# Performance work log

Measured on AMD Instinct MI355X. Metric: run time of the kernel, lower is better.

## Reference

```python
import jax, jax.numpy as jnp
import numpy as np

EPSILON = 0.1
ALPHA = 0.5
N_ITER = 10
B, N, D, N_USERS = 4096, 4096, 16, 100000


def setup_inputs() -> dict:
    key = jax.random.key(0)
    k1, k2, k3, k4, k5, k6 = jax.random.split(key, 6)
    users_tensor = jax.random.randint(k1, (B,), 0, N_USERS)
    pois_tensor = jax.random.randint(k2, (B, N), 0, N)
    D_tensor = jax.random.uniform(k3, (B, N), dtype=jnp.float32)
    # ScaledEmbedding: normal init scaled by 1/embedding_dim
    poi_emb = jax.random.normal(k4, (N, D), dtype=jnp.float32) / D
    user_emb = jax.random.normal(k5, (N_USERS, D), dtype=jnp.float32) / D
    capacities = jax.random.uniform(k6, (N,), dtype=jnp.float32) + 0.5
    return {"users_tensor": users_tensor, "pois_tensor": pois_tensor,
            "D_tensor": D_tensor, "poi_emb": poi_emb,
            "user_emb": user_emb, "capacities": capacities}


def reference(users_tensor, pois_tensor, D_tensor, poi_emb, user_emb, capacities):
    pe = poi_emb[pois_tensor]            # [B, N, D]
    ue = user_emb[users_tensor]          # [B, D]
    dot = jnp.einsum('bnd,bd->bn', pe, ue)   # [B, N]
    affinity = (1.0 - ALPHA) * dot - ALPHA * (D_tensor / jnp.mean(D_tensor))
    K = jnp.exp(affinity / EPSILON)      # [B, N]
    a = jnp.ones((B,), dtype=K.dtype)
    b = capacities

    def body(i, uv):
        u, v = uv
        u = a / (K @ v)        # [B]
        v = b / (K.T @ u)      # [N]
        return (u, v)

    u0 = jnp.ones((B,), dtype=K.dtype)
    v0 = jnp.ones((N,), dtype=K.dtype)
    u, v = jax.lax.fori_loop(0, N_ITER, body, (u0, v0))
    P = K * (u[:, None] * v[None, :])    # [B, N]
    return P
```

## Files before the change

kernel.cpp:

```cpp
#include <hip/hip_runtime.h>
#include <hip/hip_fp16.h>

#define BB 4096
#define NN 4096
#define RPB 4
#define RPI 8
#define NBLK (BB / RPI)
#define NTSLOT 60

__device__ __forceinline__ int swzK(int bid) { return (bid & 7) * 128 + (bid >> 3); }

typedef float vf4 __attribute__((ext_vector_type(4)));
typedef int   vi4 __attribute__((ext_vector_type(4)));
__device__ __forceinline__ float4 ntl4(const float4* p) {
    vf4 r = __builtin_nontemporal_load((const vf4*)p);
    return *(float4*)&r;
}
__device__ __forceinline__ int4 ntl4i(const int4* p) {
    vi4 r = __builtin_nontemporal_load((const vi4*)p);
    return *(int4*)&r;
}
__device__ __forceinline__ void nts4(float4* p, float4 v) {
    __builtin_nontemporal_store(*(vf4*)&v, (vf4*)p);
}

__global__ __launch_bounds__(256) void k_mean(
        const float* __restrict__ Dt, float* __restrict__ dsum,
        float* __restrict__ v) {
    const int tid = blockIdx.x * blockDim.x + threadIdx.x;
    const int gs = gridDim.x * blockDim.x;
    if (tid < NN) v[tid] = 1.0f;
    const float4* D4 = (const float4*)Dt;
    const int total4 = (BB * NN) / 4;
    float s = 0.f;
    for (int i = tid; i < total4; i += gs) {
        float4 d = ntl4(&D4[i]);
        s += (d.x + d.y) + (d.z + d.w);
    }
    #pragma unroll
    for (int off = 32; off > 0; off >>= 1) s += __shfl_down(s, off, 64);
    __shared__ float ls[4];
    if ((threadIdx.x & 63) == 0) ls[threadIdx.x >> 6] = s;
    __syncthreads();
    if (threadIdx.x == 0) atomicAdd(dsum, (ls[0] + ls[1]) + (ls[2] + ls[3]));
}

__global__ __launch_bounds__(256) void k_K(
        const int* __restrict__ users, const int* __restrict__ pois,
        const float* __restrict__ Dt, const float* __restrict__ poi_emb,
        const float* __restrict__ user_emb, const float* __restrict__ dsum,
        __half* __restrict__ K) {
    __shared__ __half slut[RPB][NN];
    __shared__ float ues[RPB * 16];
    const int t = threadIdx.x;
    const int b0 = swzK(blockIdx.x) * RPB;
    if (t < RPB * 16) {
        int r = t >> 4, d = t & 15;
        ues[t] = user_emb[(size_t)users[b0 + r] * 16 + d];
    }
    __syncthreads();
    float ue[RPB][16];
    #pragma unroll
    for (int r = 0; r < RPB; r++)
        #pragma unroll
        for (int d = 0; d < 16; d++) ue[r][d] = ues[r * 16 + d];

    const float4* pe4 = (const float4*)poi_emb;
    for (int j = t; j < NN; j += 256) {
        float4 p0 = pe4[j * 4 + 0];
        float4 p1 = pe4[j * 4 + 1];
        float4 p2 = pe4[j * 4 + 2];
        float4 p3 = pe4[j * 4 + 3];
        #pragma unroll
        for (int r = 0; r < RPB; r++) {
            float acc = p0.x*ue[r][0]  + p0.y*ue[r][1]  + p0.z*ue[r][2]  + p0.w*ue[r][3]
                      + p1.x*ue[r][4]  + p1.y*ue[r][5]  + p1.z*ue[r][6]  + p1.w*ue[r][7]
                      + p2.x*ue[r][8]  + p2.y*ue[r][9]  + p2.z*ue[r][10] + p2.w*ue[r][11]
                      + p3.x*ue[r][12] + p3.y*ue[r][13] + p3.z*ue[r][14] + p3.w*ue[r][15];
            slut[r][j] = __float2half(acc);
        }
    }
    __syncthreads();
    const float cc = 5.0f * 16777216.0f / dsum[0];
    #pragma unroll
    for (int r = 0; r < RPB; r++) {
        const size_t base = (size_t)(b0 + r) * NN;
        const int4*   p4 = (const int4*)(pois + base);
        const float4* d4 = (const float4*)(Dt + base);
        #pragma unroll
        for (int i = 0; i < NN / 4 / 256; i++) {
            const int q = t + i * 256;
            int4   ci = ntl4i(&p4[q]);
            float4 cd = ntl4(&d4[q]);
            float k0 = __expf(5.0f * __half2float(slut[r][ci.x]) - cc * cd.x);
            float k1 = __expf(5.0f * __half2float(slut[r][ci.y]) - cc * cd.y);
            float k2 = __expf(5.0f * __half2float(slut[r][ci.z]) - cc * cd.z);
            float k3 = __expf(5.0f * __half2float(slut[r][ci.w]) - cc * cd.w);
            __half2* kw = (__half2*)&K[base + 4 * (size_t)q];
            kw[0] = __floats2half2_rn(k0, k1);
            kw[1] = __floats2half2_rn(k2, k3);
        }
    }
}

__global__ __launch_bounds__(512) void k_it(
        const __half* __restrict__ K, const float* __restrict__ v,
        float* __restrict__ part, float* __restrict__ u) {
    const int t = threadIdx.x;
    const int slot = blockIdx.x >> 3;
    const int sb = (blockIdx.x & 7) * 64 + slot;
    const int r0 = sb * RPI;
    const bool nt = (slot >= NTSLOT);

    const float4* w4 = (const float4*)v;
    float4 w0 = w4[2 * t], w1 = w4[2 * t + 1];

    float4 h[RPI];
    #pragma unroll
    for (int r = 0; r < RPI; r++) {
        const float4* p = (const float4*)(K + (size_t)(r0 + r) * NN) + t;
        h[r] = nt ? ntl4(p) : *p;
    }

    float acc[RPI];
    #pragma unroll
    for (int r = 0; r < RPI; r++) {
        const __half2* a = (const __half2*)&h[r];
        float2 f; float s = 0.f;
        f = __half22float2(a[0]); s += f.x * w0.x + f.y * w0.y;
        f = __half22float2(a[1]); s += f.x * w0.z + f.y * w0.w;
        f = __half22float2(a[2]); s += f.x * w1.x + f.y * w1.y;
        f = __half22float2(a[3]); s += f.x * w1.z + f.y * w1.w;
        acc[r] = s;
    }
    #pragma unroll
    for (int off = 32; off > 0; off >>= 1)
        #pragma unroll
        for (int r = 0; r < RPI; r++) acc[r] += __shfl_down(acc[r], off, 64);
    __shared__ float ls[8][RPI];
    __shared__ float us[RPI];
    if ((t & 63) == 0)
        #pragma unroll
        for (int r = 0; r < RPI; r++) ls[t >> 6][r] = acc[r];
    __syncthreads();
    if (t < RPI) {
        float s = 0.f;
        #pragma unroll
        for (int wv = 0; wv < 8; wv++) s += ls[wv][t];
        float uu = 1.0f / s;
        us[t] = uu;
        u[r0 + t] = uu;
    }
    __syncthreads();

    float4 A0 = make_float4(0, 0, 0, 0), A1 = A0;
    #pragma unroll
    for (int r = 0; r < RPI; r++) {
        const float ur = us[r];
        const __half2* a = (const __half2*)&h[r];
        float2 f;
        f = __half22float2(a[0]); A0.x += ur * f.x; A0.y += ur * f.y;
        f = __half22float2(a[1]); A0.z += ur * f.x; A0.w += ur * f.y;
        f = __half22float2(a[2]); A1.x += ur * f.x; A1.y += ur * f.y;
        f = __half22float2(a[3]); A1.z += ur * f.x; A1.w += ur * f.y;
    }
    float4* p4 = (float4*)(part + (size_t)sb * NN);
    nts4(&p4[2 * t],     A0);
    nts4(&p4[2 * t + 1], A1);
}

__global__ __launch_bounds__(256) void k_red(
        const float* __restrict__ part, const float* __restrict__ cap,
        float* __restrict__ v) {
    const int t = threadIdx.x;
    const int g = blockIdx.x;
    const int j = t & 7;
    const int s = t >> 3;
    const float4* p4 = (const float4*)part;
    float4 a = make_float4(0, 0, 0, 0);
    #pragma unroll
    for (int i = 0; i < NBLK / 32; i++) {
        float4 x = ntl4(&p4[(size_t)(s + 32 * i) * (NN / 4) + g * 8 + j]);
        a.x += x.x; a.y += x.y; a.z += x.z; a.w += x.w;
    }
    __shared__ float4 red[32][8];
    red[s][j] = a;
    __syncthreads();
    if (t < 8) {
        float4 b = red[0][t];
        #pragma unroll
        for (int s2 = 1; s2 < 32; s2++) {
            float4 x = red[s2][t];
            b.x += x.x; b.y += x.y; b.z += x.z; b.w += x.w;
        }
        float4 cc = ((const float4*)cap)[g * 8 + t];
        ((float4*)v)[g * 8 + t] =
            make_float4(cc.x / b.x, cc.y / b.y, cc.z / b.z, cc.w / b.w);
    }
}

__global__ __launch_bounds__(256) void k_P(
        const __half* __restrict__ K, const float* __restrict__ u,
        const float* __restrict__ v, float* __restrict__ P) {
    const int t = threadIdx.x;
    const int slot = blockIdx.x >> 3;
    const int sb = (blockIdx.x & 7) * 64 + slot;
    const int r0 = sb * RPI;
    const bool nt = (slot >= NTSLOT);
    const float4* v4 = (const float4*)v;
    float4 va0 = v4[2 * t],       va1 = v4[2 * t + 1];
    float4 vb0 = v4[512 + 2 * t], vb1 = v4[512 + 2 * t + 1];
    #pragma unroll 2
    for (int r = 0; r < RPI; r++) {
        const int b = r0 + r;
        const float ub = u[b];
        const size_t base = (size_t)b * NN;
        const float4* k4 = (const float4*)(K + base);
        float4 raw0 = nt ? ntl4(&k4[t])       : k4[t];
        float4 raw1 = nt ? ntl4(&k4[256 + t]) : k4[256 + t];
        const __half2* ha = (const __half2*)&raw0;
        const __half2* hb = (const __half2*)&raw1;
        float2 f0 = __half22float2(ha[0]);
        float2 f1 = __half22float2(ha[1]);
        float2 f2 = __half22float2(ha[2]);
        float2 f3 = __half22float2(ha[3]);
        float2 g0 = __half22float2(hb[0]);
        float2 g1 = __half22float2(hb[1]);
        float2 g2 = __half22float2(hb[2]);
        float2 g3 = __half22float2(hb[3]);
        float4* P4 = (float4*)(P + base);
        nts4(&P4[2*t],       make_float4(f0.x*ub*va0.x, f0.y*ub*va0.y, f1.x*ub*va0.z, f1.y*ub*va0.w));
        nts4(&P4[2*t+1],     make_float4(f2.x*ub*va1.x, f2.y*ub*va1.y, f3.x*ub*va1.z, f3.y*ub*va1.w));
        nts4(&P4[512+2*t],   make_float4(g0.x*ub*vb0.x, g0.y*ub*vb0.y, g1.x*ub*vb0.z, g1.y*ub*vb0.w));
        nts4(&P4[512+2*t+1], make_float4(g2.x*ub*vb1.x, g2.y*ub*vb1.y, g3.x*ub*vb1.z, g3.y*ub*vb1.w));
    }
}

extern "C" void kernel_launch(void* const* d_in, const int* in_sizes, int n_in,
                              void* d_out, int out_size, void* d_ws, size_t ws_size,
                              hipStream_t stream) {
    const int*   users    = (const int*)d_in[0];
    const int*   pois     = (const int*)d_in[1];
    const float* Dt       = (const float*)d_in[2];
    const float* poi_emb  = (const float*)d_in[3];
    const float* user_emb = (const float*)d_in[4];
    const float* cap      = (const float*)d_in[5];
    float* out = (float*)d_out;

    float*  wsf  = (float*)d_ws;
    float*  dsum = wsf;
    float*  u    = wsf + 64;
    float*  v    = wsf + 64 + BB;
    __half* Kh   = (__half*)(wsf + 64 + BB + NN);
    float*  part = (float*)d_out;

    (void)hipMemsetAsync(dsum, 0, sizeof(float), stream);
    k_mean<<<2048, 256, 0, stream>>>(Dt, dsum, v);
    k_K<<<BB / RPB, 256, 0, stream>>>(users, pois, Dt, poi_emb, user_emb, dsum, Kh);
    for (int it = 0; it < 10; it++) {
        k_it<<<NBLK, 512, 0, stream>>>(Kh, v, part, u);
        k_red<<<128, 256, 0, stream>>>(part, cap, v);
    }
    k_P<<<NBLK, 256, 0, stream>>>(Kh, u, v, out);
}
```

Before: 372.0 us.

## Store an FP8 copy of K for the Sinkhorn iterations

The K-building kernel now writes a second, FP8-encoded copy of K (scaled by 16) into spare output memory. The iteration kernel reads this FP8 copy instead of the half-precision one, halving the bytes streamed per iteration, and it folds the scale factor into u. The cost is an extra write during construction and lower precision in the iterative matrix-vector products, which may shift u and v. The non-temporal load heuristic is also removed.

```diff
diff --git a/kernel.cpp b/kernel.cpp
--- a/kernel.cpp
+++ b/kernel.cpp
@@ -12,6 +12,7 @@
 
 typedef float vf4 __attribute__((ext_vector_type(4)));
 typedef int   vi4 __attribute__((ext_vector_type(4)));
+typedef float fv2 __attribute__((ext_vector_type(2)));
 __device__ __forceinline__ float4 ntl4(const float4* p) {
     vf4 r = __builtin_nontemporal_load((const vf4*)p);
     return *(float4*)&r;
@@ -22,6 +23,12 @@
 }
 __device__ __forceinline__ void nts4(float4* p, float4 v) {
     __builtin_nontemporal_store(*(vf4*)&v, (vf4*)p);
+}
+
+__device__ __forceinline__ void dec4(int w, float* f) {
+    fv2 lo = __builtin_amdgcn_cvt_pk_f32_fp8(w, false);
+    fv2 hi = __builtin_amdgcn_cvt_pk_f32_fp8(w, true);
+    f[0] = lo.x; f[1] = lo.y; f[2] = hi.x; f[3] = hi.y;
 }
 
 __global__ __launch_bounds__(256) void k_mean(
@@ -49,7 +56,7 @@
         const int* __restrict__ users, const int* __restrict__ pois,
         const float* __restrict__ Dt, const float* __restrict__ poi_emb,
         const float* __restrict__ user_emb, const float* __restrict__ dsum,
-        __half* __restrict__ K) {
+        __half* __restrict__ K, unsigned char* __restrict__ K8) {
     __shared__ __half slut[RPB][NN];
     __shared__ float ues[RPB * 16];
     const int t = threadIdx.x;
@@ -99,39 +106,36 @@
             __half2* kw = (__half2*)&K[base + 4 * (size_t)q];
             kw[0] = __floats2half2_rn(k0, k1);
             kw[1] = __floats2half2_rn(k2, k3);
+            int w8 = __builtin_amdgcn_cvt_pk_fp8_f32(16.f * k0, 16.f * k1, 0, false);
+            w8 = __builtin_amdgcn_cvt_pk_fp8_f32(16.f * k2, 16.f * k3, w8, true);
+            ((int*)(K8 + base))[q] = w8;
         }
     }
 }
 
 __global__ __launch_bounds__(512) void k_it(
-        const __half* __restrict__ K, const float* __restrict__ v,
+        const unsigned char* __restrict__ K8, const float* __restrict__ v,
         float* __restrict__ part, float* __restrict__ u) {
     const int t = threadIdx.x;
-    const int slot = blockIdx.x >> 3;
-    const int sb = (blockIdx.x & 7) * 64 + slot;
+    const int sb = (blockIdx.x & 7) * 64 + (blockIdx.x >> 3);
     const int r0 = sb * RPI;
-    const bool nt = (slot >= NTSLOT);
 
     const float4* w4 = (const float4*)v;
     float4 w0 = w4[2 * t], w1 = w4[2 * t + 1];
 
-    float4 h[RPI];
+    uint2 h8[RPI];
+    #pragma unroll
+    for (int r = 0; r < RPI; r++)
+        h8[r] = ((const uint2*)(K8 + (size_t)(r0 + r) * NN))[t];
+
+    float acc[RPI];
     #pragma unroll
     for (int r = 0; r < RPI; r++) {
-        const float4* p = (const float4*)(K + (size_t)(r0 + r) * NN) + t;
-        h[r] = nt ? ntl4(p) : *p;
-    }
-
-    float acc[RPI];
-    #pragma unroll
-    for (int r = 0; r < RPI; r++) {
-        const __half2* a = (const __half2*)&h[r];
-        float2 f; float s = 0.f;
-        f = __half22float2(a[0]); s += f.x * w0.x + f.y * w0.y;
-        f = __half22float2(a[1]); s += f.x * w0.z + f.y * w0.w;
-        f = __half22float2(a[2]); s += f.x * w1.x + f.y * w1.y;
-        f = __half22float2(a[3]); s += f.x * w1.z + f.y * w1.w;
-        acc[r] = s;
+        float f[8];
+        dec4((int)h8[r].x, f);
+        dec4((int)h8[r].y, f + 4);
+        acc[r] = f[0]*w0.x + f[1]*w0.y + f[2]*w0.z + f[3]*w0.w
+               + f[4]*w1.x + f[5]*w1.y + f[6]*w1.z + f[7]*w1.w;
     }
     #pragma unroll
     for (int off = 32; off > 0; off >>= 1)
@@ -149,7 +153,7 @@
         for (int wv = 0; wv < 8; wv++) s += ls[wv][t];
         float uu = 1.0f / s;
         us[t] = uu;
-        u[r0 + t] = uu;
+        u[r0 + t] = 16.0f * uu;
     }
     __syncthreads();
 
@@ -157,12 +161,11 @@
     #pragma unroll
     for (int r = 0; r < RPI; r++) {
         const float ur = us[r];
-        const __half2* a = (const __half2*)&h[r];
-        float2 f;
-        f = __half22float2(a[0]); A0.x += ur * f.x; A0.y += ur * f.y;
-        f = __half22float2(a[1]); A0.z += ur * f.x; A0.w += ur * f.y;
-        f = __half22float2(a[2]); A1.x += ur * f.x; A1.y += ur * f.y;
-        f = __half22float2(a[3]); A1.z += ur * f.x; A1.w += ur * f.y;
+        float f[8];
+        dec4((int)h8[r].x, f);
+        dec4((int)h8[r].y, f + 4);
+        A0.x += ur * f[0]; A0.y += ur * f[1]; A0.z += ur * f[2]; A0.w += ur * f[3];
+        A1.x += ur * f[4]; A1.y += ur * f[5]; A1.z += ur * f[6]; A1.w += ur * f[7];
     }
     float4* p4 = (float4*)(part + (size_t)sb * NN);
     nts4(&p4[2 * t],     A0);
@@ -253,12 +256,13 @@
     float*  v    = wsf + 64 + BB;
     __half* Kh   = (__half*)(wsf + 64 + BB + NN);
     float*  part = (float*)d_out;
+    unsigned char* K8 = (unsigned char*)(part + (size_t)NBLK * NN);
 
     (void)hipMemsetAsync(dsum, 0, sizeof(float), stream);
     k_mean<<<2048, 256, 0, stream>>>(Dt, dsum, v);
-    k_K<<<BB / RPB, 256, 0, stream>>>(users, pois, Dt, poi_emb, user_emb, dsum, Kh);
+    k_K<<<BB / RPB, 256, 0, stream>>>(users, pois, Dt, poi_emb, user_emb, dsum, Kh, K8);
     for (int it = 0; it < 10; it++) {
-        k_it<<<NBLK, 512, 0, stream>>>(Kh, v, part, u);
+        k_it<<<NBLK, 512, 0, stream>>>(K8, v, part, u);
         k_red<<<128, 256, 0, stream>>>(part, cap, v);
     }
     k_P<<<NBLK, 256, 0, stream>>>(Kh, u, v, out);
```

After: 372.8 us. About the same (+0.2%).
